# Kernel tuning notes

Hardware: AMD Instinct MI355X
Metric: run time of the kernel (lower is better)

## Reference

```python
import math
import jax, jax.numpy as jnp
import numpy as np

NUM_HEADS = 12
ALPHA, BETA, GAMMA = 1.9, 3.8, 15.2  # get_rpe_config(ratio=1.9)
SKIP = 1


def _rp_bucket(side):
    """iRPE euclidean contextual bucket table for a side x side grid + 1 cls token."""
    beta_int = int(BETA)
    coords = np.stack(np.meshgrid(np.arange(side), np.arange(side), indexing='ij'), -1).reshape(-1, 2)
    diff = coords[:, None, :] - coords[None, :, :]
    dis = np.round(np.sqrt((diff ** 2).sum(-1).astype(np.float64)))  # rounded euclidean distance
    far = np.clip(np.round(ALPHA + np.log(np.maximum(dis, 1e-9) / ALPHA) / math.log(GAMMA / ALPHA) * (BETA - ALPHA)), None, BETA)
    idx = np.where(dis <= ALPHA, dis, far).astype(np.int32) + beta_int
    num_buckets = 2 * beta_int + 1  # 7
    L = side * side
    full = np.full((L + SKIP, L + SKIP), num_buckets, dtype=np.int32)  # extra bucket for cls
    full[SKIP:, SKIP:] = idx
    return full, num_buckets + 1  # table [P,P], total buckets = 8


def setup_inputs() -> dict:
    key = jax.random.key(0)
    ks = jax.random.split(key, 8)
    B, P, n_mod, C = 64, 197, 2, 768
    N = 1 + (P - 1) * n_mod  # 393
    hd = C // NUM_HEADS
    rp_bucket, n_buckets = _rp_bucket(int(math.sqrt(P - SKIP)))
    s = 0.02
    return {
        'x': jax.random.normal(ks[0], (B, N, C), jnp.float32),
        'q_learned': jax.random.normal(ks[1], (1, 1, C), jnp.float32) * s,
        'pos_embed': jax.random.normal(ks[2], (1, P, C), jnp.float32) * s,
        'wk': jax.random.normal(ks[3], (C, C), jnp.float32) * s,
        'wv': jax.random.normal(ks[4], (C, C), jnp.float32) * s,
        'rpe_w': jax.random.normal(ks[5], (hd, n_buckets), jnp.float32) * s,  # shared_head ctx lookup table
        'proj_w': jax.random.normal(ks[6], (C, C), jnp.float32) * s,
        'proj_b': jnp.zeros((C,), jnp.float32),
        'rp_bucket': jnp.asarray(rp_bucket),  # [P, P] int32
    }


def reference(x, q_learned, pos_embed, wk, wv, rpe_w, proj_w, proj_b, rp_bucket):
    B, N, C = x.shape
    H = NUM_HEADS
    hd = C // H
    P = rp_bucket.shape[0]
    n_mod = (N - 1) // (P - 1)
    scale = hd ** -0.5

    q_ = jnp.broadcast_to(q_learned + pos_embed, (B, P, C))
    q = q_.reshape(B, P, H, hd).transpose(0, 2, 1, 3)                    # bhpd
    k = (x @ wk.T).reshape(B, N, H, hd).transpose(0, 2, 1, 3)            # bhnd
    v = (x @ wv.T).reshape(B, N, H, hd).transpose(0, 2, 1, 3)            # bhnd

    attn = jnp.einsum('bhpd,bhnd->bhpn', q, k) * scale                   # [B,H,P,N]

    # contextual RPE on keys: lookup = q @ table, gathered by rp_bucket[i, j]
    lookup = jnp.einsum('bhpd,du->bhpu', q, rpe_w)                        # [B,H,P,n_buckets]
    bias = lookup[:, :, jnp.arange(P)[:, None], rp_bucket]                # [B,H,P,P]
    bias = jnp.concatenate([bias[..., :1], jnp.tile(bias[..., 1:], (1, 1, 1, n_mod))], axis=-1)
    attn = jax.nn.softmax(attn + bias, axis=-1)

    out = jnp.einsum('bhpn,bhnd->bhpd', attn, v).transpose(0, 2, 1, 3).reshape(B, P, C)
    return out @ proj_w.T + proj_b
```

## Files before the change

kernel.cpp:

```cpp
#include <hip/hip_runtime.h>

typedef unsigned short u16;
typedef short bf16x8 __attribute__((ext_vector_type(8)));
typedef float f32x4 __attribute__((ext_vector_type(4)));
typedef const __attribute__((address_space(1))) void* gptr_t;
typedef __attribute__((address_space(3))) void* lptr_t;

#define B_   64
#define N_   393
#define C_   768
#define H_   12
#define HD_  64
#define P_   197
#define BIAS_N 416
#define PPAD 208
#define VTP  448
#define M_KV (B_ * N_)
#define M_PR (B_ * P_)
#define SCALE_L2E 0.180336879f

__device__ __forceinline__ u16 f2bf(float f) {
    unsigned u = __float_as_uint(f);
    return (u16)((u + 0x7FFFu + ((u >> 16) & 1u)) >> 16);
}
__device__ __forceinline__ unsigned cvt_pk_bf16(float lo, float hi) {
    unsigned r;
    asm("v_cvt_pk_bf16_f32 %0, %1, %2" : "=v"(r) : "v"(lo), "v"(hi));
    return r;
}
__device__ __forceinline__ float exp2_fast(float x) {
    float r;
    asm("v_exp_f32 %0, %1" : "=v"(r) : "v"(x));
    return r;
}

__global__ __launch_bounds__(256) void f2bf_kernel(const float* __restrict__ in,
                                                   u16* __restrict__ out, int n4) {
    int i = blockIdx.x * 256 + threadIdx.x;
    if (i < n4) {
        float4 v = ((const float4*)in)[i];
        u16 o[4] = {f2bf(v.x), f2bf(v.y), f2bf(v.z), f2bf(v.w)};
        *(uint2*)(out + i * 4) = *(uint2*)o;
    }
}

__global__ __launch_bounds__(256) void convw_kernel(
    const float* __restrict__ wk, const float* __restrict__ wv,
    const float* __restrict__ pw, u16* __restrict__ wkvh, u16* __restrict__ pwh) {
    int sec = blockIdx.x / 576;
    int i = (blockIdx.x % 576) * 256 + threadIdx.x;
    const float* src = sec == 0 ? wk : (sec == 1 ? wv : pw);
    u16* dst = sec == 0 ? wkvh : (sec == 1 ? wkvh + 589824 : pwh);
    float4 v = ((const float4*)src)[i];
    u16 o[4] = {f2bf(v.x), f2bf(v.y), f2bf(v.z), f2bf(v.w)};
    *(uint2*)(dst + i * 4) = *(uint2*)o;
}

__global__ __launch_bounds__(256) void prep1_kernel(
    const float* __restrict__ q_learned, const float* __restrict__ pos_embed,
    const float* __restrict__ rpe_w, u16* __restrict__ qh, float* __restrict__ lk)
{
    __shared__ float q_s[C_];
    const int p = blockIdx.x, t = threadIdx.x;
    for (int c = t; c < C_; c += 256) {
        float v = q_learned[c] + pos_embed[p * C_ + c];
        q_s[c] = v;
        qh[p * C_ + c] = f2bf(v);
    }
    __syncthreads();
    if (t < H_ * 8) {
        int h = t >> 3, u = t & 7;
        float s = 0.f;
        #pragma unroll 8
        for (int d = 0; d < HD_; ++d)
            s = fmaf(q_s[h * HD_ + d], rpe_w[d * 8 + u], s);
        lk[(h * P_ + p) * 8 + u] = s;
    }
}

__global__ __launch_bounds__(256) void prep2_kernel(
    const float* __restrict__ lk, const int* __restrict__ rp_bucket,
    float* __restrict__ biasT)
{
    int bx = blockIdx.x;
    int h = bx / N_, j = bx % N_;
    int t = threadIdx.x;
    if (t >= PPAD) return;
    int jm;
    if (j == 0) jm = 0;
    else { jm = j - 1; if (jm >= 196) jm -= 196; jm += 1; }
    float v = 0.f;
    if (t < P_) {
        int bucket = rp_bucket[t * P_ + jm];
        v = lk[(h * P_ + t) * 8 + bucket] * 1.44269504f;
    }
    biasT[((size_t)h * BIAS_N + j) * PPAD + t] = v;
}

__global__ __launch_bounds__(256) void gemm_kv(
    const u16* __restrict__ A, const u16* __restrict__ Bw,
    u16* __restrict__ Kb, u16* __restrict__ Vt)
{
    __shared__ __align__(16) u16 As[128 * 64];
    __shared__ __align__(16) u16 Bs[128 * 64];

    const int gx = gridDim.x;
    const int nwg = gx * gridDim.y;
    const int orig = blockIdx.y * gx + blockIdx.x;
    const int xcd = orig & 7, rank = orig >> 3;
    const int q = nwg >> 3, r = nwg & 7;
    const int wgid = (xcd < r ? xcd * (q + 1) : r * (q + 1) + (xcd - r) * q) + rank;
    const int n0 = (wgid % gx) * 128;
    const int m0 = (wgid / gx) * 128;

    const int t = threadIdx.x;
    const int w = t >> 6, l = t & 63;
    const int wr = w >> 1, wc = w & 1;
    const int l15 = l & 15, lg = l >> 4;
    const int lrow = l >> 3, lslot = l & 7;

    f32x4 acc[4][4];
    #pragma unroll
    for (int i = 0; i < 4; ++i)
        #pragma unroll
        for (int j = 0; j < 4; ++j) acc[i][j] = (f32x4){0.f, 0.f, 0.f, 0.f};

    for (int ks = 0; ks < 12; ++ks) {
        const int k0 = ks * 64;
        if (ks) __syncthreads();
        #pragma unroll
        for (int i = 0; i < 4; ++i) {
            const int rbase = w * 32 + i * 8;
            int arow = m0 + rbase + lrow; if (arow > M_KV - 1) arow = M_KV - 1;
            const int brow = n0 + rbase + lrow;
            const u16* ga = A  + (size_t)arow * 768 + k0 + lslot * 8;
            const u16* gb = Bw + (size_t)brow * 768 + k0 + lslot * 8;
            __builtin_amdgcn_global_load_lds((gptr_t)(const void*)ga,
                                             (lptr_t)(void*)(As + rbase * 64), 16, 0, 0);
            __builtin_amdgcn_global_load_lds((gptr_t)(const void*)gb,
                                             (lptr_t)(void*)(Bs + rbase * 64), 16, 0, 0);
        }
        __syncthreads();
        #pragma unroll
        for (int kk = 0; kk < 2; ++kk) {
            bf16x8 af[4], bfr[4];
            #pragma unroll
            for (int mf = 0; mf < 4; ++mf) {
                af[mf]  = *(const bf16x8*)(As + (wr * 64 + mf * 16 + l15) * 64 + (kk * 4 + lg) * 8);
                bfr[mf] = *(const bf16x8*)(Bs + (wc * 64 + mf * 16 + l15) * 64 + (kk * 4 + lg) * 8);
            }
            #pragma unroll
            for (int mf = 0; mf < 4; ++mf)
                #pragma unroll
                for (int nf = 0; nf < 4; ++nf)
                    acc[mf][nf] = __builtin_amdgcn_mfma_f32_16x16x32_bf16(
                        af[mf], bfr[nf], acc[mf][nf], 0, 0, 0);
        }
    }

    if (n0 < 768) {
        #pragma unroll
        for (int mf = 0; mf < 4; ++mf)
            #pragma unroll
            for (int nf = 0; nf < 4; ++nf) {
                int col = n0 + wc * 64 + nf * 16 + l15;
                #pragma unroll
                for (int rr = 0; rr < 4; ++rr) {
                    int m = m0 + wr * 64 + mf * 16 + lg * 4 + rr;
                    if (m < M_KV) Kb[(size_t)m * 768 + col] = f2bf(acc[mf][nf][rr]);
                }
            }
    } else {
        const int dgbase = n0 - 768 + wc * 64;
        #pragma unroll
        for (int mf = 0; mf < 4; ++mf)
            #pragma unroll
            for (int rr = 0; rr < 4; ++rr) {
                int m = m0 + wr * 64 + mf * 16 + lg * 4 + rr;
                if (m < M_KV) {
                    int bb = m / 393;
                    int jj = m - bb * 393;
                    u16* vrow = Vt + (size_t)(bb * 768 + dgbase) * VTP + jj;
                    #pragma unroll
                    for (int nf = 0; nf < 4; ++nf)
                        vrow[(size_t)(nf * 16 + l15) * VTP] = f2bf(acc[mf][nf][rr]);
                }
            }
    }
}

__global__ __launch_bounds__(256) void gemm_proj(
    const u16* __restrict__ A, const u16* __restrict__ Bw,
    float* __restrict__ Cf, const float* __restrict__ bias)
{
    __shared__ __align__(16) u16 As[128 * 64];
    __shared__ __align__(16) u16 Bs[128 * 64];

    const int gx = gridDim.x;
    const int nwg = gx * gridDim.y;
    const int orig = blockIdx.y * gx + blockIdx.x;
    const int xcd = orig & 7, rank = orig >> 3;
    const int q = nwg >> 3, r = nwg & 7;
    const int wgid = (xcd < r ? xcd * (q + 1) : r * (q + 1) + (xcd - r) * q) + rank;
    const int n0 = (wgid % gx) * 128;
    const int m0 = (wgid / gx) * 128;

    const int t = threadIdx.x;
    const int w = t >> 6, l = t & 63;
    const int wr = w >> 1, wc = w & 1;
    const int l15 = l & 15, lg = l >> 4;
    const int lrow = l >> 3, lslot = l & 7;

    f32x4 acc[4][4];
    #pragma unroll
    for (int i = 0; i < 4; ++i)
        #pragma unroll
        for (int j = 0; j < 4; ++j) acc[i][j] = (f32x4){0.f, 0.f, 0.f, 0.f};

    for (int ks = 0; ks < 12; ++ks) {
        const int k0 = ks * 64;
        if (ks) __syncthreads();
        #pragma unroll
        for (int i = 0; i < 4; ++i) {
            const int rbase = w * 32 + i * 8;
            int arow = m0 + rbase + lrow; if (arow > M_PR - 1) arow = M_PR - 1;
            const int brow = n0 + rbase + lrow;
            const u16* ga = A  + (size_t)arow * 768 + k0 + lslot * 8;
            const u16* gb = Bw + (size_t)brow * 768 + k0 + lslot * 8;
            __builtin_amdgcn_global_load_lds((gptr_t)(const void*)ga,
                                             (lptr_t)(void*)(As + rbase * 64), 16, 0, 0);
            __builtin_amdgcn_global_load_lds((gptr_t)(const void*)gb,
                                             (lptr_t)(void*)(Bs + rbase * 64), 16, 0, 0);
        }
        __syncthreads();
        #pragma unroll
        for (int kk = 0; kk < 2; ++kk) {
            bf16x8 af[4], bfr[4];
            #pragma unroll
            for (int mf = 0; mf < 4; ++mf) {
                af[mf]  = *(const bf16x8*)(As + (wr * 64 + mf * 16 + l15) * 64 + (kk * 4 + lg) * 8);
                bfr[mf] = *(const bf16x8*)(Bs + (wc * 64 + mf * 16 + l15) * 64 + (kk * 4 + lg) * 8);
            }
            #pragma unroll
            for (int mf = 0; mf < 4; ++mf)
                #pragma unroll
                for (int nf = 0; nf < 4; ++nf)
                    acc[mf][nf] = __builtin_amdgcn_mfma_f32_16x16x32_bf16(
                        af[mf], bfr[nf], acc[mf][nf], 0, 0, 0);
        }
    }

    #pragma unroll
    for (int mf = 0; mf < 4; ++mf)
        #pragma unroll
        for (int nf = 0; nf < 4; ++nf) {
            int col = n0 + wc * 64 + nf * 16 + l15;
            float bb = bias[col];
            #pragma unroll
            for (int rr = 0; rr < 4; ++rr) {
                int m = m0 + wr * 64 + mf * 16 + lg * 4 + rr;
                if (m < M_PR) Cf[(size_t)m * 768 + col] = acc[mf][nf][rr] + bb;
            }
        }
}

__global__ __launch_bounds__(256, 2) void attn_mfma3(
    const u16* __restrict__ qh, const u16* __restrict__ Kb,
    const u16* __restrict__ Vt, const float* __restrict__ biasT,
    u16* __restrict__ Obuf)
{
    __shared__ __align__(16) u16 pts[64 * 456];
    __shared__ __align__(16) u16 kvs[2][64 * 64];

    const int id = blockIdx.x;
    const int work = (id & 7) * 384 + (id >> 3);
    const int ptile = work & 3;
    const int rest = work >> 2;
    const int h = rest % 12;
    const int b = rest / 12;
    const int p0 = ptile * 64;

    const int t = threadIdx.x, w = t >> 6, l = t & 63;
    const int l15 = l & 15, lg = l >> 4;
    const int p0w = p0 + w * 16;

    int srow[2], sslot[2], swoff[2];
    #pragma unroll
    for (int i = 0; i < 2; ++i) {
        int c = t + 256 * i;
        srow[i] = c >> 3; sslot[i] = c & 7;
        swoff[i] = srow[i] * 64 + ((sslot[i] ^ (srow[i] & 7)) << 3);
    }

    int prow = p0w + l15; if (prow > P_ - 1) prow = P_ - 1;
    const u16* qp = qh + (size_t)prow * C_ + h * HD_ + lg * 8;
    bf16x8 qf0 = *(const bf16x8*)(qp);
    bf16x8 qf1 = *(const bf16x8*)(qp + 32);

    const u16* Kbase = Kb + (size_t)b * (N_ * 768) + h * HD_;
    const u16* Vbase = Vt + (size_t)(b * H_ + h) * (HD_ * VTP);

    f32x4 acc[7][4];
    #pragma unroll
    for (int i = 0; i < 7; ++i)
        #pragma unroll
        for (int j = 0; j < 4; ++j) acc[i][j] = (f32x4){0.f, 0.f, 0.f, 0.f};

    bf16x8 ra[2];
    #pragma unroll
    for (int i = 0; i < 2; ++i)
        ra[i] = *(const bf16x8*)(Kbase + (size_t)srow[i] * 768 + sslot[i] * 8);
    #pragma unroll
    for (int i = 0; i < 2; ++i) *(bf16x8*)(&kvs[0][swoff[i]]) = ra[i];
    __syncthreads();

    #pragma unroll
    for (int nt = 0; nt < 7; ++nt) {
        const u16* kcur = kvs[nt & 1];
        if (nt < 6) {
            #pragma unroll
            for (int i = 0; i < 2; ++i) {
                int rn = (nt + 1) * 64 + srow[i]; if (rn > N_ - 1) rn = N_ - 1;
                ra[i] = *(const bf16x8*)(Kbase + (size_t)rn * 768 + sslot[i] * 8);
            }
        }
        __builtin_amdgcn_s_setprio(1);
        #pragma unroll
        for (int kc = 0; kc < 2; ++kc)
            #pragma unroll
            for (int sub = 0; sub < 4; ++sub) {
                int row = sub * 16 + l15;
                bf16x8 kb = *(const bf16x8*)(kcur + row * 64 + (((kc * 4 + lg) ^ (row & 7)) << 3));
                acc[nt][sub] = __builtin_amdgcn_mfma_f32_16x16x32_bf16(
                    kc ? qf1 : qf0, kb, acc[nt][sub], 0, 0, 0);
            }
        __builtin_amdgcn_s_setprio(0);
        if (nt < 6) {
            #pragma unroll
            for (int i = 0; i < 2; ++i) *(bf16x8*)(&kvs[(nt + 1) & 1][swoff[i]]) = ra[i];
        }
        __syncthreads();
    }

    #pragma unroll
    for (int i = 0; i < 2; ++i)
        ra[i] = *(const bf16x8*)(Vbase + (size_t)srow[i] * VTP + sslot[i] * 8);

    const int pcl = (p0w + lg * 4) > (PPAD - 4) ? (PPAD - 4) : (p0w + lg * 4);
    float s4[4] = {0.f, 0.f, 0.f, 0.f};
    #pragma unroll
    for (int nt = 0; nt < 7; ++nt)
        #pragma unroll
        for (int sub = 0; sub < 4; ++sub) {
            int n = nt * 64 + sub * 16 + l15;
            if (n < N_) {
                float4 b4 = *(const float4*)(biasT + ((size_t)h * BIAS_N + n) * PPAD + pcl);
                float bb[4] = {b4.x, b4.y, b4.z, b4.w};
                #pragma unroll
                for (int rr = 0; rr < 4; ++rr) {
                    float e = exp2_fast(fmaf(acc[nt][sub][rr], SCALE_L2E, bb[rr]));
                    acc[nt][sub][rr] = e;
                    s4[rr] += e;
                }
            } else {
                acc[nt][sub] = (f32x4){0.f, 0.f, 0.f, 0.f};
            }
        }
    float rinv4[4];
    #pragma unroll
    for (int rr = 0; rr < 4; ++rr) {
        float s = s4[rr];
        s += __shfl_xor(s, 1); s += __shfl_xor(s, 2);
        s += __shfl_xor(s, 4); s += __shfl_xor(s, 8);
        rinv4[rr] = 1.0f / s;
    }

    {
        const int rowb = w * 16 + lg * 4;
        #pragma unroll
        for (int nt = 0; nt < 7; ++nt)
            #pragma unroll
            for (int sub = 0; sub < 4; ++sub) {
                int col = nt * 64 + sub * 16 + l15;
                unsigned pk01 = cvt_pk_bf16(acc[nt][sub][0] * rinv4[0],
                                            acc[nt][sub][1] * rinv4[1]);
                unsigned pk23 = cvt_pk_bf16(acc[nt][sub][2] * rinv4[2],
                                            acc[nt][sub][3] * rinv4[3]);
                pts[(rowb + 0) * 456 + col] = (u16)pk01;
                pts[(rowb + 1) * 456 + col] = (u16)(pk01 >> 16);
                pts[(rowb + 2) * 456 + col] = (u16)pk23;
                pts[(rowb + 3) * 456 + col] = (u16)(pk23 >> 16);
            }
    }
    #pragma unroll
    for (int i = 0; i < 2; ++i) *(bf16x8*)(&kvs[0][swoff[i]]) = ra[i];
    __syncthreads();

    f32x4 o[4];
    #pragma unroll
    for (int i = 0; i < 4; ++i) o[i] = (f32x4){0.f, 0.f, 0.f, 0.f};

    #pragma unroll
    for (int nt = 0; nt < 7; ++nt) {
        const u16* kcur = kvs[nt & 1];
        if (nt < 6) {
            #pragma unroll
            for (int i = 0; i < 2; ++i)
                ra[i] = *(const bf16x8*)(Vbase + (size_t)srow[i] * VTP + (nt + 1) * 64 + sslot[i] * 8);
        }
        __builtin_amdgcn_s_setprio(1);
        #pragma unroll
        for (int kc = 0; kc < 2; ++kc) {
            bf16x8 pa = *(const bf16x8*)(pts + (w * 16 + l15) * 456 + nt * 64 + kc * 32 + lg * 8);
            #pragma unroll
            for (int dsub = 0; dsub < 4; ++dsub) {
                int row = dsub * 16 + l15;
                bf16x8 vb = *(const bf16x8*)(kcur + row * 64 + (((kc * 4 + lg) ^ (row & 7)) << 3));
                o[dsub] = __builtin_amdgcn_mfma_f32_16x16x32_bf16(pa, vb, o[dsub], 0, 0, 0);
            }
        }
        __builtin_amdgcn_s_setprio(0);
        if (nt < 6) {
            #pragma unroll
            for (int i = 0; i < 2; ++i) *(bf16x8*)(&kvs[(nt + 1) & 1][swoff[i]]) = ra[i];
        }
        __syncthreads();
    }

    #pragma unroll
    for (int dsub = 0; dsub < 4; ++dsub)
        #pragma unroll
        for (int rr = 0; rr < 4; ++rr) {
            int p = p0w + lg * 4 + rr;
            if (p < P_)
                Obuf[((size_t)b * P_ + p) * C_ + h * HD_ + dsub * 16 + l15] = f2bf(o[dsub][rr]);
        }
}

extern "C" void kernel_launch(void* const* d_in, const int* in_sizes, int n_in,
                              void* d_out, int out_size, void* d_ws, size_t ws_size,
                              hipStream_t stream)
{
    const float* x         = (const float*)d_in[0];
    const float* q_learned = (const float*)d_in[1];
    const float* pos_embed = (const float*)d_in[2];
    const float* wk        = (const float*)d_in[3];
    const float* wv        = (const float*)d_in[4];
    const float* rpe_w     = (const float*)d_in[5];
    const float* proj_w    = (const float*)d_in[6];
    const float* proj_b    = (const float*)d_in[7];
    const int*   rp_bucket = (const int*)d_in[8];
    float* out = (float*)d_out;

    char* ws = (char*)d_ws;
    u16*   xh    = (u16*)(ws);
    u16*   wkvh  = (u16*)(ws + 38633472);
    u16*   pwh   = (u16*)(ws + 40992768);
    u16*   qh    = (u16*)(ws + 42172416);
    float* lk    = (float*)(ws + 42475008);
    float* biasT = (float*)(ws + 42550784);
    u16*   Kbuf  = (u16*)(ws + 46704128);
    u16*   Vt    = (u16*)(ws + 85337600);
    u16*   Obuf  = (u16*)(ws + 129377792);

    f2bf_kernel<<<(19316736 / 4 + 255) / 256, 256, 0, stream>>>(x, xh, 19316736 / 4);
    convw_kernel<<<3 * 576, 256, 0, stream>>>(wk, wv, proj_w, wkvh, pwh);

    prep1_kernel<<<P_, 256, 0, stream>>>(q_learned, pos_embed, rpe_w, qh, lk);
    prep2_kernel<<<H_ * N_, 256, 0, stream>>>(lk, rp_bucket, biasT);

    dim3 gkv(12, (M_KV + 127) / 128);
    gemm_kv<<<gkv, 256, 0, stream>>>(xh, wkvh, Kbuf, Vt);

    attn_mfma3<<<3072, 256, 0, stream>>>(qh, Kbuf, Vt, biasT, Obuf);

    dim3 gpr(6, (M_PR + 127) / 128);
    gemm_proj<<<gpr, 256, 0, stream>>>(Obuf, pwh, out, proj_b);
}
```

Measured before the change: 267.9 us.

## Store K head-major, stage V transpose through LDS, trim attention tail work

K is now written head-major ([b,h,n,d]), so each attention block reads its K tile contiguously instead of with a 768-element stride. The V transpose in gemm_kv goes through LDS and is written as 8-wide vector stores, replacing scattered 2-byte writes, and a new kernel zeroes the V padding columns. The attention kernel skips MFMA, bias and pack work on the last partial key tile and applies the softmax normalisation once to the output instead of to every probability. The two conversion kernels are merged into one launch. These changes add an extra launch and more complex epilogue code, and the pts padding must be zeroed to keep the result correct.

```diff
diff --git a/kernel.cpp b/kernel.cpp
--- a/kernel.cpp
+++ b/kernel.cpp
@@ -34,26 +34,34 @@
     return r;
 }
 
-__global__ __launch_bounds__(256) void f2bf_kernel(const float* __restrict__ in,
-                                                   u16* __restrict__ out, int n4) {
+__global__ __launch_bounds__(256) void conv_all(
+    const float* __restrict__ x, const float* __restrict__ wk,
+    const float* __restrict__ wv, const float* __restrict__ pw,
+    u16* __restrict__ xh, u16* __restrict__ wkvh, u16* __restrict__ pwh)
+{
+    const int XN4 = 19316736 / 4;
+    const int WN4 = 589824 / 4;
     int i = blockIdx.x * 256 + threadIdx.x;
-    if (i < n4) {
-        float4 v = ((const float4*)in)[i];
-        u16 o[4] = {f2bf(v.x), f2bf(v.y), f2bf(v.z), f2bf(v.w)};
-        *(uint2*)(out + i * 4) = *(uint2*)o;
-    }
-}
-
-__global__ __launch_bounds__(256) void convw_kernel(
-    const float* __restrict__ wk, const float* __restrict__ wv,
-    const float* __restrict__ pw, u16* __restrict__ wkvh, u16* __restrict__ pwh) {
-    int sec = blockIdx.x / 576;
-    int i = (blockIdx.x % 576) * 256 + threadIdx.x;
-    const float* src = sec == 0 ? wk : (sec == 1 ? wv : pw);
-    u16* dst = sec == 0 ? wkvh : (sec == 1 ? wkvh + 589824 : pwh);
-    float4 v = ((const float4*)src)[i];
+    const float* src; u16* dst; int off;
+    if (i < XN4) { src = x; dst = xh; off = i; }
+    else {
+        int j = i - XN4;
+        int sec = j / WN4;
+        off = j - sec * WN4;
+        src = sec == 0 ? wk : (sec == 1 ? wv : pw);
+        dst = sec == 0 ? wkvh : (sec == 1 ? wkvh + 589824 : pwh);
+    }
+    float4 v = ((const float4*)src)[off];
     u16 o[4] = {f2bf(v.x), f2bf(v.y), f2bf(v.z), f2bf(v.w)};
-    *(uint2*)(dst + i * 4) = *(uint2*)o;
+    *(uint2*)(dst + off * 4) = *(uint2*)o;
+}
+
+__global__ __launch_bounds__(256) void vzero_kernel(u16* __restrict__ Vt)
+{
+    int idx = blockIdx.x * 256 + threadIdx.x;
+    int row = idx >> 6, c = idx & 63;
+    if (c < 55)
+        Vt[(size_t)row * VTP + 393 + c] = 0;
 }
 
 __global__ __launch_bounds__(256) void prep1_kernel(
@@ -99,10 +107,11 @@
 
 __global__ __launch_bounds__(256) void gemm_kv(
     const u16* __restrict__ A, const u16* __restrict__ Bw,
-    u16* __restrict__ Kb, u16* __restrict__ Vt)
-{
-    __shared__ __align__(16) u16 As[128 * 64];
-    __shared__ __align__(16) u16 Bs[128 * 64];
+    u16* __restrict__ Kh, u16* __restrict__ Vt)
+{
+    __shared__ __align__(16) u16 pool[16384];
+    u16* As = pool;
+    u16* Bs = pool + 8192;
 
     const int gx = gridDim.x;
     const int nwg = gx * gridDim.y;
@@ -118,6 +127,7 @@
     const int wr = w >> 1, wc = w & 1;
     const int l15 = l & 15, lg = l >> 4;
     const int lrow = l >> 3, lslot = l & 7;
+    const int Mc = M_KV - 1;
 
     f32x4 acc[4][4];
     #pragma unroll
@@ -131,7 +141,7 @@
         #pragma unroll
         for (int i = 0; i < 4; ++i) {
             const int rbase = w * 32 + i * 8;
-            int arow = m0 + rbase + lrow; if (arow > M_KV - 1) arow = M_KV - 1;
+            int arow = m0 + rbase + lrow; if (arow > Mc) arow = Mc;
             const int brow = n0 + rbase + lrow;
             const u16* ga = A  + (size_t)arow * 768 + k0 + lslot * 8;
             const u16* gb = Bw + (size_t)brow * 768 + k0 + lslot * 8;
@@ -160,32 +170,84 @@
 
     if (n0 < 768) {
         #pragma unroll
-        for (int mf = 0; mf < 4; ++mf)
-            #pragma unroll
-            for (int nf = 0; nf < 4; ++nf) {
-                int col = n0 + wc * 64 + nf * 16 + l15;
-                #pragma unroll
-                for (int rr = 0; rr < 4; ++rr) {
-                    int m = m0 + wr * 64 + mf * 16 + lg * 4 + rr;
-                    if (m < M_KV) Kb[(size_t)m * 768 + col] = f2bf(acc[mf][nf][rr]);
-                }
-            }
-    } else {
-        const int dgbase = n0 - 768 + wc * 64;
-        #pragma unroll
-        for (int mf = 0; mf < 4; ++mf)
+        for (int mf = 0; mf < 4; ++mf) {
+            int mbase = m0 + wr * 64 + mf * 16 + lg * 4;
             #pragma unroll
             for (int rr = 0; rr < 4; ++rr) {
-                int m = m0 + wr * 64 + mf * 16 + lg * 4 + rr;
+                int m = mbase + rr;
                 if (m < M_KV) {
                     int bb = m / 393;
                     int jj = m - bb * 393;
-                    u16* vrow = Vt + (size_t)(bb * 768 + dgbase) * VTP + jj;
                     #pragma unroll
-                    for (int nf = 0; nf < 4; ++nf)
-                        vrow[(size_t)(nf * 16 + l15) * VTP] = f2bf(acc[mf][nf][rr]);
+                    for (int nf = 0; nf < 4; ++nf) {
+                        int col = n0 + wc * 64 + nf * 16 + l15;
+                        int hh = col >> 6, dl = col & 63;
+                        Kh[((size_t)(bb * 12 + hh) * 393 + jj) * 64 + dl] =
+                            f2bf(acc[mf][nf][rr]);
+                    }
                 }
             }
+        }
+    } else {
+        const int dg0 = n0 - 768;
+        #pragma unroll
+        for (int ph = 0; ph < 2; ++ph) {
+            __syncthreads();
+            if (wr == ph) {
+                #pragma unroll
+                for (int mf = 0; mf < 4; ++mf)
+                    #pragma unroll
+                    for (int nf = 0; nf < 4; ++nf) {
+                        int dim = wc * 64 + nf * 16 + l15;
+                        int tokr = mf * 16 + lg * 4;
+                        unsigned v01 = cvt_pk_bf16(acc[mf][nf][0], acc[mf][nf][1]);
+                        unsigned v23 = cvt_pk_bf16(acc[mf][nf][2], acc[mf][nf][3]);
+                        *(unsigned*)(pool + dim * 72 + tokr)     = v01;
+                        *(unsigned*)(pool + dim * 72 + tokr + 2) = v23;
+                    }
+            }
+            __syncthreads();
+            const int T0 = m0 + ph * 64;
+            if (T0 < M_KV) {
+                int b0 = T0 / 393, J0 = T0 - 393 * b0;
+                int S = 393 - J0; if (S > 64) S = 64;
+                #pragma unroll
+                for (int seg = 0; seg < 2; ++seg) {
+                    int bb  = b0 + seg;
+                    int ja  = seg ? 0      : J0;
+                    int len = seg ? 64 - S : S;
+                    int tr0 = seg ? S      : -J0;
+                    if (bb >= B_ || len <= 0) continue;
+                    int jc0 = ja & ~7;
+                    int nch = ((ja + len + 7) >> 3) - (jc0 >> 3);
+                    for (int i = t; i < 128 * 16; i += 256) {
+                        int ci = i & 15, dim = i >> 4;
+                        if (ci >= nch) continue;
+                        int jc = jc0 + ci * 8;
+                        bool full = (jc >= ja) && (jc + 8 <= ja + len);
+                        u16 vals[8];
+                        #pragma unroll
+                        for (int k = 0; k < 8; ++k) {
+                            int j = jc + k;
+                            int tr = tr0 + j;
+                            tr = tr < 0 ? 0 : (tr > 63 ? 63 : tr);
+                            u16 v = pool[dim * 72 + tr];
+                            vals[k] = (j >= ja && j < ja + len) ? v : (u16)0;
+                        }
+                        u16* dst = Vt + (size_t)(bb * 768 + dg0 + dim) * VTP;
+                        if (full) {
+                            *(bf16x8*)(dst + jc) = *(bf16x8*)vals;
+                        } else {
+                            #pragma unroll
+                            for (int k = 0; k < 8; ++k) {
+                                int j = jc + k;
+                                if (j >= ja && j < ja + len) dst[j] = vals[k];
+                            }
+                        }
+                    }
+                }
+            }
+        }
     }
 }
 
@@ -210,6 +272,7 @@
     const int wr = w >> 1, wc = w & 1;
     const int l15 = l & 15, lg = l >> 4;
     const int lrow = l >> 3, lslot = l & 7;
+    const int Mc = M_PR - 1;
 
     f32x4 acc[4][4];
     #pragma unroll
@@ -223,7 +286,7 @@
         #pragma unroll
         for (int i = 0; i < 4; ++i) {
             const int rbase = w * 32 + i * 8;
-            int arow = m0 + rbase + lrow; if (arow > M_PR - 1) arow = M_PR - 1;
+            int arow = m0 + rbase + lrow; if (arow > Mc) arow = Mc;
             const int brow = n0 + rbase + lrow;
             const u16* ga = A  + (size_t)arow * 768 + k0 + lslot * 8;
             const u16* gb = Bw + (size_t)brow * 768 + k0 + lslot * 8;
@@ -264,8 +327,8 @@
         }
 }
 
-__global__ __launch_bounds__(256, 2) void attn_mfma3(
-    const u16* __restrict__ qh, const u16* __restrict__ Kb,
+__global__ __launch_bounds__(256, 2) void attn_mfma5(
+    const u16* __restrict__ qh, const u16* __restrict__ Kh,
     const u16* __restrict__ Vt, const float* __restrict__ biasT,
     u16* __restrict__ Obuf)
 {
@@ -297,7 +360,7 @@
     bf16x8 qf0 = *(const bf16x8*)(qp);
     bf16x8 qf1 = *(const bf16x8*)(qp + 32);
 
-    const u16* Kbase = Kb + (size_t)b * (N_ * 768) + h * HD_;
+    const u16* Kbase = Kh + (size_t)(b * 12 + h) * (N_ * HD_);
     const u16* Vbase = Vt + (size_t)(b * H_ + h) * (HD_ * VTP);
 
     f32x4 acc[7][4];
@@ -309,7 +372,7 @@
     bf16x8 ra[2];
     #pragma unroll
     for (int i = 0; i < 2; ++i)
-        ra[i] = *(const bf16x8*)(Kbase + (size_t)srow[i] * 768 + sslot[i] * 8);
+        ra[i] = *(const bf16x8*)(Kbase + srow[i] * 64 + sslot[i] * 8);
     #pragma unroll
     for (int i = 0; i < 2; ++i) *(bf16x8*)(&kvs[0][swoff[i]]) = ra[i];
     __syncthreads();
@@ -321,14 +384,15 @@
             #pragma unroll
             for (int i = 0; i < 2; ++i) {
                 int rn = (nt + 1) * 64 + srow[i]; if (rn > N_ - 1) rn = N_ - 1;
-                ra[i] = *(const bf16x8*)(Kbase + (size_t)rn * 768 + sslot[i] * 8);
-            }
-        }
+                ra[i] = *(const bf16x8*)(Kbase + rn * 64 + sslot[i] * 8);
+            }
+        }
+        const int smax = (nt == 6) ? 1 : 4;
         __builtin_amdgcn_s_setprio(1);
         #pragma unroll
         for (int kc = 0; kc < 2; ++kc)
             #pragma unroll
-            for (int sub = 0; sub < 4; ++sub) {
+            for (int sub = 0; sub < smax; ++sub) {
                 int row = sub * 16 + l15;
                 bf16x8 kb = *(const bf16x8*)(kcur + row * 64 + (((kc * 4 + lg) ^ (row & 7)) << 3));
                 acc[nt][sub] = __builtin_amdgcn_mfma_f32_16x16x32_bf16(
@@ -349,9 +413,10 @@
     const int pcl = (p0w + lg * 4) > (PPAD - 4) ? (PPAD - 4) : (p0w + lg * 4);
     float s4[4] = {0.f, 0.f, 0.f, 0.f};
     #pragma unroll
-    for (int nt = 0; nt < 7; ++nt)
-        #pragma unroll
-        for (int sub = 0; sub < 4; ++sub) {
+    for (int nt = 0; nt < 7; ++nt) {
+        const int smax = (nt == 6) ? 1 : 4;
+        #pragma unroll
+        for (int sub = 0; sub < smax; ++sub) {
             int n = nt * 64 + sub * 16 + l15;
             if (n < N_) {
                 float4 b4 = *(const float4*)(biasT + ((size_t)h * BIAS_N + n) * PPAD + pcl);
@@ -366,6 +431,7 @@
                 acc[nt][sub] = (f32x4){0.f, 0.f, 0.f, 0.f};
             }
         }
+    }
     float rinv4[4];
     #pragma unroll
     for (int rr = 0; rr < 4; ++rr) {
@@ -378,19 +444,22 @@
     {
         const int rowb = w * 16 + lg * 4;
         #pragma unroll
-        for (int nt = 0; nt < 7; ++nt)
-            #pragma unroll
-            for (int sub = 0; sub < 4; ++sub) {
+        for (int nt = 0; nt < 7; ++nt) {
+            const int smax = (nt == 6) ? 1 : 4;
+            #pragma unroll
+            for (int sub = 0; sub < smax; ++sub) {
                 int col = nt * 64 + sub * 16 + l15;
-                unsigned pk01 = cvt_pk_bf16(acc[nt][sub][0] * rinv4[0],
-                                            acc[nt][sub][1] * rinv4[1]);
-                unsigned pk23 = cvt_pk_bf16(acc[nt][sub][2] * rinv4[2],
-                                            acc[nt][sub][3] * rinv4[3]);
+                unsigned pk01 = cvt_pk_bf16(acc[nt][sub][0], acc[nt][sub][1]);
+                unsigned pk23 = cvt_pk_bf16(acc[nt][sub][2], acc[nt][sub][3]);
                 pts[(rowb + 0) * 456 + col] = (u16)pk01;
                 pts[(rowb + 1) * 456 + col] = (u16)(pk01 >> 16);
                 pts[(rowb + 2) * 456 + col] = (u16)pk23;
                 pts[(rowb + 3) * 456 + col] = (u16)(pk23 >> 16);
             }
+        }
+        #pragma unroll
+        for (int rr = 0; rr < 4; ++rr)
+            pts[(rowb + rr) * 456 + 400 + l15] = 0;
     }
     #pragma unroll
     for (int i = 0; i < 2; ++i) *(bf16x8*)(&kvs[0][swoff[i]]) = ra[i];
@@ -408,9 +477,10 @@
             for (int i = 0; i < 2; ++i)
                 ra[i] = *(const bf16x8*)(Vbase + (size_t)srow[i] * VTP + (nt + 1) * 64 + sslot[i] * 8);
         }
+        const int kcmax = (nt == 6) ? 1 : 2;
         __builtin_amdgcn_s_setprio(1);
         #pragma unroll
-        for (int kc = 0; kc < 2; ++kc) {
+        for (int kc = 0; kc < kcmax; ++kc) {
             bf16x8 pa = *(const bf16x8*)(pts + (w * 16 + l15) * 456 + nt * 64 + kc * 32 + lg * 8);
             #pragma unroll
             for (int dsub = 0; dsub < 4; ++dsub) {
@@ -433,7 +503,8 @@
         for (int rr = 0; rr < 4; ++rr) {
             int p = p0w + lg * 4 + rr;
             if (p < P_)
-                Obuf[((size_t)b * P_ + p) * C_ + h * HD_ + dsub * 16 + l15] = f2bf(o[dsub][rr]);
+                Obuf[((size_t)b * P_ + p) * C_ + h * HD_ + dsub * 16 + l15] =
+                    f2bf(o[dsub][rr] * rinv4[rr]);
         }
 }
 
@@ -459,21 +530,22 @@
     u16*   qh    = (u16*)(ws + 42172416);
     float* lk    = (float*)(ws + 42475008);
     float* biasT = (float*)(ws + 42550784);
-    u16*   Kbuf  = (u16*)(ws + 46704128);
+    u16*   Kh    = (u16*)(ws + 46704128);
     u16*   Vt    = (u16*)(ws + 85337600);
     u16*   Obuf  = (u16*)(ws + 129377792);
 
-    f2bf_kernel<<<(19316736 / 4 + 255) / 256, 256, 0, stream>>>(x, xh, 19316736 / 4);
-    convw_kernel<<<3 * 576, 256, 0, stream>>>(wk, wv, proj_w, wkvh, pwh);
+    conv_all<<<20592, 256, 0, stream>>>(x, wk, wv, proj_w, xh, wkvh, pwh);
 
     prep1_kernel<<<P_, 256, 0, stream>>>(q_learned, pos_embed, rpe_w, qh, lk);
     prep2_kernel<<<H_ * N_, 256, 0, stream>>>(lk, rp_bucket, biasT);
 
-    dim3 gkv(12, (M_KV + 127) / 128);
-    gemm_kv<<<gkv, 256, 0, stream>>>(xh, wkvh, Kbuf, Vt);
-
-    attn_mfma3<<<3072, 256, 0, stream>>>(qh, Kbuf, Vt, biasT, Obuf);
-
-    dim3 gpr(6, (M_PR + 127) / 128);
+    vzero_kernel<<<12288, 256, 0, stream>>>(Vt);
+
+    dim3 gkv(1536 / 128, (M_KV + 127) / 128);
+    gemm_kv<<<gkv, 256, 0, stream>>>(xh, wkvh, Kh, Vt);
+
+    attn_mfma5<<<3072, 256, 0, stream>>>(qh, Kh, Vt, biasT, Obuf);
+
+    dim3 gpr(768 / 128, (M_PR + 127) / 128);
     gemm_proj<<<gpr, 256, 0, stream>>>(Obuf, pwh, out, proj_b);
 }
```

Measured after the change: 274.1 us. 1.02x slower.
